# Kernel optimization log

Measured on AMD Instinct MI355X. Metric: run time of the kernel, lower is better.

## Reference

```python
import jax, jax.numpy as jnp
import numpy as np

B, C, H, W = 8, 512, 64, 64
KD, VD, OD = 64, 512, 512
BN_EPS = 1e-5


def setup_inputs() -> dict:
    key = jax.random.key(0)
    ks = jax.random.split(key, 10)
    s = lambda fan_in: 1.0 / np.sqrt(fan_in)
    return {
        "x": jax.random.normal(ks[0], (B, C, H, W), jnp.float32),
        "Wq": jax.random.normal(ks[1], (KD, C), jnp.float32) * s(C),
        "bq": jnp.zeros((KD,), jnp.float32),
        "Wk": jax.random.normal(ks[2], (KD, C), jnp.float32) * s(C),
        "bk": jnp.zeros((KD,), jnp.float32),
        "Wv": jax.random.normal(ks[3], (VD, C), jnp.float32) * s(C),
        "bv": jnp.zeros((VD,), jnp.float32),
        "gamma": jnp.zeros((1,), jnp.float32),  # torch init: zeros(1)
        "Wf": jax.random.normal(ks[4], (OD, VD), jnp.float32) * s(VD),
        "bn_w": jnp.ones((OD,), jnp.float32),
        "bn_b": jnp.zeros((OD,), jnp.float32),
        "bn_mean": jnp.zeros((OD,), jnp.float32),
        "bn_var": jnp.ones((OD,), jnp.float32),
    }


def reference(x, Wq, bq, Wk, bk, Wv, bv, gamma, Wf, bn_w, bn_b, bn_mean, bn_var):
    b, c, h, w = x.shape
    n = h * w
    # 1x1 convs == per-pixel channel matmuls
    q = jnp.einsum('bchw,kc->bkhw', x, Wq) + bq[None, :, None, None]  # [B,KD,H,W]
    k = jnp.einsum('bchw,kc->bkhw', x, Wk) + bk[None, :, None, None]
    v = jnp.einsum('bchw,vc->bvhw', x, Wv) + bv[None, :, None, None]
    q = q.reshape(b, -1, n)  # [B,KD,N]
    k = k.reshape(b, -1, n)
    v = v.reshape(b, -1, n)  # [B,VD,N]
    # energy[b, i, j] = q[:, :, i] . k[:, :, j]   (proj_query permuted)
    energy = jnp.einsum('bki,bkj->bij', q, k)  # [B,N,N]
    attention = jax.nn.softmax(energy, axis=-1)
    # out = value @ attention^T : out[b, v, i] = sum_j value[b, v, j] * attention[b, i, j]
    out = jnp.einsum('bvj,bij->bvi', v, attention)  # [B,VD,N]
    out = out.reshape(b, c, h, w)
    out = gamma * out + x
    # fuse: 1x1 conv (no bias) -> BatchNorm (inference) -> ReLU
    fused = jnp.einsum('bchw,oc->bohw', out, Wf)
    inv = jax.lax.rsqrt(bn_var + BN_EPS)
    fused = (fused - bn_mean[None, :, None, None]) * (bn_w * inv)[None, :, None, None] + bn_b[None, :, None, None]
    return jax.nn.relu(fused)
```

## Files before the change

### kernel.cpp

```cpp
#include <hip/hip_runtime.h>
#include <hip/hip_bf16.h>

typedef unsigned short u16;
typedef unsigned int u32;
typedef __attribute__((ext_vector_type(8))) short bf16x8;
typedef __attribute__((ext_vector_type(4))) float f32x4;
typedef __attribute__((ext_vector_type(4))) u16 u16x4;

#define B_ 8
#define C_ 512
#define N_ 4096
#define KD_ 64
#define VD_ 512
#define OD_ 512

static __device__ __forceinline__ float bf2f(u16 u) {
    union { u32 i; float f; } z; z.i = ((u32)u) << 16; return z.f;
}
static __device__ __forceinline__ u16 f2bf(float f) {
    union { float f; u32 u; } v; v.f = f;
    u32 r = v.u + 0x7fffu + ((v.u >> 16) & 1u);
    return (u16)(r >> 16);
}

__global__ __launch_bounds__(256) void transpose_convert_kernel(
    const float* __restrict__ x, const float* __restrict__ Wf,
    u16* __restrict__ xT, u16* __restrict__ Wf16)
{
    const int bid = blockIdx.x;
    if (bid >= 4096) {
        const int tid = (bid - 4096) * 256 + threadIdx.x;
        const float4* src = (const float4*)Wf + (size_t)tid * 16;
        u16* dst = Wf16 + (size_t)tid * 64;
        #pragma unroll
        for (int j = 0; j < 16; j++) {
            const float4 f = src[j];
            u16x4 p;
            p[0] = f2bf(f.x); p[1] = f2bf(f.y); p[2] = f2bf(f.z); p[3] = f2bf(f.w);
            *(u16x4*)(dst + j * 4) = p;
        }
        return;
    }
    __shared__ u32 tile[64][33];
    const int nt = bid & 63;
    const int ct = (bid >> 6) & 7;
    const int b  = bid >> 9;
    const float* xb  = x  + ((size_t)b * C_ + ct * 64) * N_ + nt * 64;
    u16*         xTb = xT + ((size_t)b * N_ + nt * 64) * C_ + ct * 64;
    const int t = threadIdx.x;
    {
        const int p  = t >> 3;
        const int n8 = t & 7;
        const float* r0 = xb + (size_t)(2 * p)     * N_ + n8 * 8;
        const float* r1 = xb + (size_t)(2 * p + 1) * N_ + n8 * 8;
        const float4 a0 = *(const float4*)(r0);
        const float4 a1 = *(const float4*)(r0 + 4);
        const float4 c0 = *(const float4*)(r1);
        const float4 c1 = *(const float4*)(r1 + 4);
        const float av[8] = { a0.x, a0.y, a0.z, a0.w, a1.x, a1.y, a1.z, a1.w };
        const float cv[8] = { c0.x, c0.y, c0.z, c0.w, c1.x, c1.y, c1.z, c1.w };
        #pragma unroll
        for (int j = 0; j < 8; j++)
            tile[n8 * 8 + j][p] = (u32)f2bf(av[j]) | ((u32)f2bf(cv[j]) << 16);
    }
    __syncthreads();
    #pragma unroll
    for (int h = 0; h < 2; h++) {
        const int id = t + h * 256;
        const int n  = id >> 3;
        const int q  = id & 7;
        uint4 val;
        val.x = tile[n][q * 4 + 0];
        val.y = tile[n][q * 4 + 1];
        val.z = tile[n][q * 4 + 2];
        val.w = tile[n][q * 4 + 3];
        *(uint4*)(xTb + (size_t)n * C_ + q * 8) = val;
    }
}

__global__ __launch_bounds__(256) void proj_kernel(
    const u16* __restrict__ xT,
    const float* __restrict__ Wq, const float* __restrict__ bq,
    const float* __restrict__ Wk, const float* __restrict__ bk,
    const float* __restrict__ Wv, const float* __restrict__ bv,
    const float* __restrict__ gamma,
    u16* __restrict__ q, u16* __restrict__ k, u16* __restrict__ v)
{
    if (gamma[0] == 0.0f) return;
    const int b = blockIdx.x >> 6;
    const int p = (blockIdx.x & 63) * 64 + (threadIdx.x & 63);
    const int dg = threadIdx.x >> 6;
    const u16* xrow = xT + ((size_t)b * N_ + p) * C_;
    for (int d0 = dg * 160; d0 < dg * 160 + 160; d0++) {
        const float* wrow; float bias; u16* dst; int dd; int dim;
        if (d0 < 64)       { dd = d0;       wrow = Wq + (size_t)dd * C_; bias = bq[dd]; dst = q; dim = KD_; }
        else if (d0 < 128) { dd = d0 - 64;  wrow = Wk + (size_t)dd * C_; bias = bk[dd]; dst = k; dim = KD_; }
        else               { dd = d0 - 128; wrow = Wv + (size_t)dd * C_; bias = bv[dd]; dst = v; dim = VD_; }
        float s = bias;
        for (int c = 0; c < C_; c++) s += bf2f(xrow[c]) * wrow[c];
        dst[((size_t)b * dim + dd) * N_ + p] = f2bf(s);
    }
}

__global__ __launch_bounds__(256) void attn_kernel(
    const u16* __restrict__ xT, const u16* __restrict__ q,
    const u16* __restrict__ k, const u16* __restrict__ v,
    const float* __restrict__ gamma, u16* __restrict__ yT)
{
    const float g = gamma[0];
    if (g == 0.0f) return;
    __shared__ float pls[4][64];
    const int wv = threadIdx.x >> 6, lane = threadIdx.x & 63;
    const int b  = blockIdx.x >> 7;
    const int q0 = (blockIdx.x & 127) * 32 + wv * 8;
    const u16* kb = k + (size_t)b * KD_ * N_;
    const u16* vb = v + (size_t)b * VD_ * N_;
    for (int qi = 0; qi < 8; qi++) {
        const int i = q0 + qi;
        const float qv = bf2f(q[((size_t)b * KD_ + lane) * N_ + i]);
        float mx = -1e30f, l = 0.f;
        for (int jb = 0; jb < N_; jb += 64) {
            float e = 0.f;
            for (int kd = 0; kd < 64; kd++)
                e += __shfl(qv, kd) * bf2f(kb[(size_t)kd * N_ + jb + lane]);
            const float nm = fmaxf(mx, e);
            l = l * __expf(mx - nm) + __expf(e - nm);
            mx = nm;
        }
        for (int off = 32; off; off >>= 1) {
            const float mo = __shfl_xor(mx, off);
            const float lo = __shfl_xor(l, off);
            const float nm = fmaxf(mx, mo);
            l = l * __expf(mx - nm) + lo * __expf(mo - nm);
            mx = nm;
        }
        float oacc[8];
        #pragma unroll
        for (int r = 0; r < 8; r++) oacc[r] = 0.f;
        for (int jb = 0; jb < N_; jb += 64) {
            float e = 0.f;
            for (int kd = 0; kd < 64; kd++)
                e += __shfl(qv, kd) * bf2f(kb[(size_t)kd * N_ + jb + lane]);
            __syncthreads();
            pls[wv][lane] = __expf(e - mx);
            __syncthreads();
            for (int jj = 0; jj < 64; jj++) {
                const float p = pls[wv][jj];
                #pragma unroll
                for (int r = 0; r < 8; r++)
                    oacc[r] += p * bf2f(vb[(size_t)(r * 64 + lane) * N_ + jb + jj]);
            }
        }
        const float inv = 1.f / l;
        #pragma unroll
        for (int r = 0; r < 8; r++) {
            const size_t idx = ((size_t)b * N_ + i) * C_ + r * 64 + lane;
            yT[idx] = f2bf(g * oacc[r] * inv + bf2f(xT[idx]));
        }
    }
}

__global__ __launch_bounds__(256) void gemm_bn_relu(
    const u16* __restrict__ xT, const u16* __restrict__ yT,
    const u16* __restrict__ Wf16, const float* __restrict__ gamma,
    const float* __restrict__ bnw, const float* __restrict__ bnb,
    const float* __restrict__ bnm, const float* __restrict__ bnv,
    float* __restrict__ out)
{
    constexpr int LP = 40;
    __shared__ u16 lds_x[128 * LP];
    __shared__ u16 lds_w[128 * LP];

    const int bid = blockIdx.x;
    const int ot = bid & 3;
    const int pt = (bid >> 2) & 31;
    const int b  = bid >> 7;

    const u16* src = (gamma[0] != 0.0f) ? yT : xT;
    const u16* Xb = src + ((size_t)b * N_ + pt * 128) * (size_t)C_;
    const u16* Wb = Wf16 + (size_t)(ot * 128) * C_;

    const int t = threadIdx.x;
    const int row_a = t >> 2;
    const int off_a = (t & 3) << 3;

    const int lane = t & 63;
    const int wv = t >> 6;
    const int wm = wv >> 1;
    const int wn = wv & 1;
    const int lcol = lane & 15;
    const int kq = lane >> 4;

    f32x4 acc[4][4];
    #pragma unroll
    for (int i = 0; i < 4; i++)
        #pragma unroll
        for (int j = 0; j < 4; j++)
            acc[i][j] = (f32x4){0.f, 0.f, 0.f, 0.f};

    uint4 rx0 = *(const uint4*)(Xb + (size_t)row_a * C_ + off_a);
    uint4 rx1 = *(const uint4*)(Xb + (size_t)(row_a + 64) * C_ + off_a);
    uint4 rw0 = *(const uint4*)(Wb + (size_t)row_a * C_ + off_a);
    uint4 rw1 = *(const uint4*)(Wb + (size_t)(row_a + 64) * C_ + off_a);

    for (int ks = 0; ks < 16; ks++) {
        __syncthreads();
        *(uint4*)&lds_x[row_a * LP + off_a]        = rx0;
        *(uint4*)&lds_x[(row_a + 64) * LP + off_a] = rx1;
        *(uint4*)&lds_w[row_a * LP + off_a]        = rw0;
        *(uint4*)&lds_w[(row_a + 64) * LP + off_a] = rw1;
        if (ks < 15) {
            const int k0 = (ks + 1) << 5;
            rx0 = *(const uint4*)(Xb + (size_t)row_a * C_ + k0 + off_a);
            rx1 = *(const uint4*)(Xb + (size_t)(row_a + 64) * C_ + k0 + off_a);
            rw0 = *(const uint4*)(Wb + (size_t)row_a * C_ + k0 + off_a);
            rw1 = *(const uint4*)(Wb + (size_t)(row_a + 64) * C_ + k0 + off_a);
        }
        __syncthreads();
        bf16x8 af[4], bfg[4];
        #pragma unroll
        for (int mi = 0; mi < 4; mi++)
            af[mi] = *(const bf16x8*)&lds_x[(wm * 64 + mi * 16 + lcol) * LP + kq * 8];
        #pragma unroll
        for (int ni = 0; ni < 4; ni++)
            bfg[ni] = *(const bf16x8*)&lds_w[(wn * 64 + ni * 16 + lcol) * LP + kq * 8];
        #pragma unroll
        for (int mi = 0; mi < 4; mi++)
            #pragma unroll
            for (int ni = 0; ni < 4; ni++)
                acc[mi][ni] = __builtin_amdgcn_mfma_f32_16x16x32_bf16(
                    af[mi], bfg[ni], acc[mi][ni], 0, 0, 0);
    }

    float scale[4], shift[4];
    #pragma unroll
    for (int ni = 0; ni < 4; ni++) {
        const int o = ot * 128 + wn * 64 + ni * 16 + lcol;
        const float s = bnw[o] * rsqrtf(bnv[o] + 1e-5f);
        scale[ni] = s;
        shift[ni] = bnb[o] - bnm[o] * s;
    }
    #pragma unroll
    for (int mi = 0; mi < 4; mi++) {
        const int npix = pt * 128 + wm * 64 + mi * 16 + kq * 4;
        #pragma unroll
        for (int ni = 0; ni < 4; ni++) {
            const int o = ot * 128 + wn * 64 + ni * 16 + lcol;
            f32x4 pk;
            #pragma unroll
            for (int r = 0; r < 4; r++)
                pk[r] = fmaxf(acc[mi][ni][r] * scale[ni] + shift[ni], 0.0f);
            *(f32x4*)(out + ((size_t)b * OD_ + o) * N_ + npix) = pk;
        }
    }
}

extern "C" void kernel_launch(void* const* d_in, const int* in_sizes, int n_in,
                              void* d_out, int out_size, void* d_ws, size_t ws_size,
                              hipStream_t stream) {
    const float* x     = (const float*)d_in[0];
    const float* Wq    = (const float*)d_in[1];
    const float* bq    = (const float*)d_in[2];
    const float* Wk    = (const float*)d_in[3];
    const float* bk    = (const float*)d_in[4];
    const float* Wv    = (const float*)d_in[5];
    const float* bv    = (const float*)d_in[6];
    const float* gamma = (const float*)d_in[7];
    const float* Wf    = (const float*)d_in[8];
    const float* bnw   = (const float*)d_in[9];
    const float* bnb   = (const float*)d_in[10];
    const float* bnm   = (const float*)d_in[11];
    const float* bnv   = (const float*)d_in[12];
    float* out = (float*)d_out;

    char* ws = (char*)d_ws;
    u16* xT   = (u16*)(ws);
    u16* Wf16 = (u16*)(ws + 33554432);
    u16* yT   = (u16*)(ws + 34078720);
    u16* q    = (u16*)(ws + 67633152);
    u16* k    = (u16*)(ws + 71827456);
    u16* v    = (u16*)(ws + 76021760);

    transpose_convert_kernel<<<4112, 256, 0, stream>>>(x, Wf, xT, Wf16);
    proj_kernel<<<512, 256, 0, stream>>>(xT, Wq, bq, Wk, bk, Wv, bv, gamma, q, k, v);
    attn_kernel<<<1024, 256, 0, stream>>>(xT, q, k, v, gamma, yT);
    gemm_bn_relu<<<1024, 256, 0, stream>>>(xT, yT, Wf16, gamma, bnw, bnb, bnm, bnv, out);
}
```

Baseline: 170.6 us.

## Swizzle LDS layout, deepen X prefetch, and regroup blocks in fused GEMM

Reworks the final 1x1-conv GEMM with BN and ReLU. The padded LDS rows are replaced by an XOR-swizzled unpadded layout to avoid bank conflicts. Two X k-slices are now kept in flight in registers, block indices are remapped so neighbouring blocks share X tiles across output tiles for L2 reuse, and launch bounds request 4 blocks per CU. This costs more registers, and the attention kernel, which likely dominates the runtime, is unchanged.

```diff
diff --git a/kernel.cpp b/kernel.cpp
--- a/kernel.cpp
+++ b/kernel.cpp
@@ -160,29 +160,35 @@
     }
 }
 
-__global__ __launch_bounds__(256) void gemm_bn_relu(
+__global__ __launch_bounds__(256, 4) void gemm_bn_relu(
     const u16* __restrict__ xT, const u16* __restrict__ yT,
     const u16* __restrict__ Wf16, const float* __restrict__ gamma,
     const float* __restrict__ bnw, const float* __restrict__ bnb,
     const float* __restrict__ bnm, const float* __restrict__ bnv,
     float* __restrict__ out)
 {
-    constexpr int LP = 40;
-    __shared__ u16 lds_x[128 * LP];
-    __shared__ u16 lds_w[128 * LP];
+    __shared__ u16 lds_x[128 * 32];
+    __shared__ u16 lds_w[128 * 32];
 
     const int bid = blockIdx.x;
-    const int ot = bid & 3;
-    const int pt = (bid >> 2) & 31;
-    const int b  = bid >> 7;
+    const int pt8 = bid & 7;
+    const int ot  = (bid >> 3) & 3;
+    const int g   = bid >> 5;
+    const int pt  = (g & 3) * 8 + pt8;
+    const int b   = g >> 2;
 
     const u16* src = (gamma[0] != 0.0f) ? yT : xT;
     const u16* Xb = src + ((size_t)b * N_ + pt * 128) * (size_t)C_;
     const u16* Wb = Wf16 + (size_t)(ot * 128) * C_;
 
     const int t = threadIdx.x;
-    const int row_a = t >> 2;
-    const int off_a = (t & 3) << 3;
+    const int r0 = t >> 2;
+    const int p  = t & 3;
+    const int q  = p ^ (r0 & 3);
+    const int wx0 = r0 * 32 + p * 8;
+    const int wx1 = wx0 + 64 * 32;
+    const size_t gx0 = (size_t)r0 * C_ + q * 8;
+    const size_t gx1 = (size_t)(r0 + 64) * C_ + q * 8;
 
     const int lane = t & 63;
     const int wv = t >> 6;
@@ -190,6 +196,7 @@
     const int wn = wv & 1;
     const int lcol = lane & 15;
     const int kq = lane >> 4;
+    const int sw = (kq ^ (lcol & 3)) * 8;
 
     f32x4 acc[4][4];
     #pragma unroll
@@ -198,38 +205,58 @@
         for (int j = 0; j < 4; j++)
             acc[i][j] = (f32x4){0.f, 0.f, 0.f, 0.f};
 
-    uint4 rx0 = *(const uint4*)(Xb + (size_t)row_a * C_ + off_a);
-    uint4 rx1 = *(const uint4*)(Xb + (size_t)(row_a + 64) * C_ + off_a);
-    uint4 rw0 = *(const uint4*)(Wb + (size_t)row_a * C_ + off_a);
-    uint4 rw1 = *(const uint4*)(Wb + (size_t)(row_a + 64) * C_ + off_a);
-
-    for (int ks = 0; ks < 16; ks++) {
-        __syncthreads();
-        *(uint4*)&lds_x[row_a * LP + off_a]        = rx0;
-        *(uint4*)&lds_x[(row_a + 64) * LP + off_a] = rx1;
-        *(uint4*)&lds_w[row_a * LP + off_a]        = rw0;
-        *(uint4*)&lds_w[(row_a + 64) * LP + off_a] = rw1;
-        if (ks < 15) {
-            const int k0 = (ks + 1) << 5;
-            rx0 = *(const uint4*)(Xb + (size_t)row_a * C_ + k0 + off_a);
-            rx1 = *(const uint4*)(Xb + (size_t)(row_a + 64) * C_ + k0 + off_a);
-            rw0 = *(const uint4*)(Wb + (size_t)row_a * C_ + k0 + off_a);
-            rw1 = *(const uint4*)(Wb + (size_t)(row_a + 64) * C_ + k0 + off_a);
-        }
-        __syncthreads();
+    auto compute = [&]() {
         bf16x8 af[4], bfg[4];
         #pragma unroll
         for (int mi = 0; mi < 4; mi++)
-            af[mi] = *(const bf16x8*)&lds_x[(wm * 64 + mi * 16 + lcol) * LP + kq * 8];
+            af[mi] = *(const bf16x8*)&lds_x[(wm * 64 + mi * 16 + lcol) * 32 + sw];
         #pragma unroll
         for (int ni = 0; ni < 4; ni++)
-            bfg[ni] = *(const bf16x8*)&lds_w[(wn * 64 + ni * 16 + lcol) * LP + kq * 8];
+            bfg[ni] = *(const bf16x8*)&lds_w[(wn * 64 + ni * 16 + lcol) * 32 + sw];
         #pragma unroll
         for (int mi = 0; mi < 4; mi++)
             #pragma unroll
             for (int ni = 0; ni < 4; ni++)
                 acc[mi][ni] = __builtin_amdgcn_mfma_f32_16x16x32_bf16(
                     af[mi], bfg[ni], acc[mi][ni], 0, 0, 0);
+    };
+
+    uint4 xa0 = *(const uint4*)(Xb + gx0);
+    uint4 xa1 = *(const uint4*)(Xb + gx1);
+    uint4 xb0 = *(const uint4*)(Xb + gx0 + 32);
+    uint4 xb1 = *(const uint4*)(Xb + gx1 + 32);
+    uint4 w0  = *(const uint4*)(Wb + gx0);
+    uint4 w1  = *(const uint4*)(Wb + gx1);
+
+    for (int ks = 0; ks < 16; ks += 2) {
+        __syncthreads();
+        *(uint4*)&lds_x[wx0] = xa0;
+        *(uint4*)&lds_x[wx1] = xa1;
+        *(uint4*)&lds_w[wx0] = w0;
+        *(uint4*)&lds_w[wx1] = w1;
+        if (ks + 2 < 16) {
+            xa0 = *(const uint4*)(Xb + gx0 + (ks + 2) * 32);
+            xa1 = *(const uint4*)(Xb + gx1 + (ks + 2) * 32);
+        }
+        w0 = *(const uint4*)(Wb + gx0 + (ks + 1) * 32);
+        w1 = *(const uint4*)(Wb + gx1 + (ks + 1) * 32);
+        __syncthreads();
+        compute();
+        __syncthreads();
+        *(uint4*)&lds_x[wx0] = xb0;
+        *(uint4*)&lds_x[wx1] = xb1;
+        *(uint4*)&lds_w[wx0] = w0;
+        *(uint4*)&lds_w[wx1] = w1;
+        if (ks + 3 < 16) {
+            xb0 = *(const uint4*)(Xb + gx0 + (ks + 3) * 32);
+            xb1 = *(const uint4*)(Xb + gx1 + (ks + 3) * 32);
+        }
+        if (ks + 2 < 16) {
+            w0 = *(const uint4*)(Wb + gx0 + (ks + 2) * 32);
+            w1 = *(const uint4*)(Wb + gx1 + (ks + 2) * 32);
+        }
+        __syncthreads();
+        compute();
     }
 
     float scale[4], shift[4];
```

Measured after the change: 166.8 us. 1.02x faster.
